# Kernel tuning notes

Measured on AMD Instinct MI355X. Metric: run time of the kernel, lower is better.

The kernel has to match this reference:

```python
import jax, jax.numpy as jnp
import numpy as np

WS = 8      # window size
NH = 8      # num heads
ED = 256    # embed dim
HD = ED // NH  # head dim


def conv2d(x, w, b):
    # x: [B,C,H,W], w: [O,I,3,3] (torch OIHW), SAME padding, stride 1
    y = jax.lax.conv_general_dilated(x, w, (1, 1), 'SAME',
                                     dimension_numbers=('NCHW', 'OIHW', 'NCHW'))
    return y + b[None, :, None, None]


def linear(x, w, b):
    # torch Linear: y = x @ W^T + b, w: [out,in]
    return jnp.einsum('bnc,oc->bno', x, w) + b


def window_partition(x, ws):
    B, C, H, W = x.shape
    x = x.reshape(B, C, H // ws, ws, W // ws, ws)
    x = jnp.transpose(x, (0, 2, 4, 3, 5, 1))  # B, H/ws, W/ws, ws, ws, C
    return x.reshape(-1, ws * ws, C)


def window_reverse(win, H, W, ws, C):
    nW = (H // ws) * (W // ws)
    B = win.shape[0] // nW
    x = win.reshape(B, H // ws, W // ws, ws, ws, C)
    x = jnp.transpose(x, (0, 5, 1, 3, 2, 4))
    return x.reshape(B, C, H, W)


def setup_inputs() -> dict:
    key = jax.random.key(0)
    ks = jax.random.split(key, 24)
    s = 0.02
    inp = {
        'xmap': jax.random.normal(ks[0], (4, ED, 256, 256), jnp.float32),
        'xfeat': jax.random.normal(ks[1], (4, 32, 256, 256), jnp.float32),
        'cmap_w': jax.random.normal(ks[2], (ED, ED, 3, 3), jnp.float32) * s,
        'cmap_b': jnp.zeros((ED,), jnp.float32),
        'cfeat_w': jax.random.normal(ks[3], (ED, 32, 3, 3), jnp.float32) * s,
        'cfeat_b': jnp.zeros((ED,), jnp.float32),
        'qxmap_w': jax.random.normal(ks[4], (ED, ED), jnp.float32) * s,
        'qxmap_b': jnp.zeros((ED,), jnp.float32),
        'kxmap_w': jax.random.normal(ks[5], (ED, ED), jnp.float32) * s,
        'kxmap_b': jnp.zeros((ED,), jnp.float32),
        'vxmap_w': jax.random.normal(ks[6], (ED, ED), jnp.float32) * s,
        'vxmap_b': jnp.zeros((ED,), jnp.float32),
        'qxfeat_w': jax.random.normal(ks[7], (ED, ED), jnp.float32) * s,
        'qxfeat_b': jnp.zeros((ED,), jnp.float32),
        'kxfeat_w': jax.random.normal(ks[8], (ED, ED), jnp.float32) * s,
        'kxfeat_b': jnp.zeros((ED,), jnp.float32),
        'proj_w': jax.random.normal(ks[9], (ED, ED), jnp.float32) * s,
        'proj_b': jnp.zeros((ED,), jnp.float32),
        'cout_w': jax.random.normal(ks[10], (ED, ED, 3, 3), jnp.float32) * s,
        'cout_b': jnp.zeros((ED,), jnp.float32),
    }
    return inp


def reference(xmap, xfeat, cmap_w, cmap_b, cfeat_w, cfeat_b,
              qxmap_w, qxmap_b, kxmap_w, kxmap_b, vxmap_w, vxmap_b,
              qxfeat_w, qxfeat_b, kxfeat_w, kxfeat_b,
              proj_w, proj_b, cout_w, cout_b):
    B, C, H, W = xmap.shape  # xfeat matches spatial size -> no interpolate branch
    xmap = conv2d(xmap, cmap_w, cmap_b)
    identity = xmap
    wm = window_partition(xmap, WS)                        # [Bw, N, C]
    wf = window_partition(conv2d(xfeat, cfeat_w, cfeat_b), WS)
    Bw, N, _ = wm.shape

    def heads(t):
        return jnp.transpose(t.reshape(Bw, N, NH, HD), (0, 2, 1, 3))  # [Bw,H,N,D]

    q_m = heads(linear(wm, qxmap_w, qxmap_b))
    k_m = heads(linear(wm, kxmap_w, kxmap_b))
    v_m = heads(linear(wm, vxmap_w, vxmap_b))
    q_f = heads(linear(wf, qxfeat_w, qxfeat_b))
    k_f = heads(linear(wf, kxfeat_w, kxfeat_b))

    q_g = jax.nn.sigmoid(q_f) * q_m
    k_g = jax.nn.sigmoid(k_f) * k_m

    scale = 1.0 / jnp.sqrt(jnp.asarray(HD, q_g.dtype))
    attn = jax.nn.softmax(jnp.einsum('bhnd,bhmd->bhnm', q_g, k_g) * scale, axis=-1)
    out = jnp.einsum('bhnm,bhmd->bhnd', attn, v_m)         # [Bw,H,N,D]
    out = jnp.transpose(out, (0, 2, 1, 3)).reshape(Bw, N, C)
    out = window_reverse(linear(out, proj_w, proj_b), H, W, WS, C)
    return conv2d(out, cout_w, cout_b) + identity
```

## Files before the change

kernel.cpp:

```cpp
#include <hip/hip_runtime.h>
#include <hip/hip_bf16.h>
#include <cstdint>
#include <math.h>

using bf16 = __hip_bfloat16;
typedef __attribute__((ext_vector_type(4))) float f32x4;
typedef __attribute__((ext_vector_type(8))) short s16x8;
typedef __attribute__((ext_vector_type(4))) short s16x4;

#define AS3(p) ((__attribute__((address_space(3))) void *)(p))
#define AS1(p) ((const __attribute__((address_space(1))) void *)(p))

static constexpr int Himg = 256, Wimg = 256, Bimg = 4;
static constexpr int HWimg = Himg * Wimg;
static constexpr int Ttok = Bimg * HWimg;

__device__ __forceinline__ void gld16(bf16* lds, const bf16* g) {
  __builtin_amdgcn_global_load_lds(AS1(g), AS3(lds), 16, 0, 0);
}

__device__ __forceinline__ unsigned short f2u(float f) {
  bf16 b = __float2bfloat16(f);
  unsigned short u; __builtin_memcpy(&u, &b, 2); return u;
}

__device__ __forceinline__ int remap_lin(int bid, int total) {
  return (bid & 7) * (total >> 3) + (bid >> 3);
}
__device__ __forceinline__ void remap_tile(int bid, int total, int NY, int BMv, int& t0, int& n0) {
  int lin = remap_lin(bid, total);
  t0 = (lin / NY) * BMv;
  n0 = (lin % NY) * 128;
}

__global__ void k_zero4k(float* p) {
  p[blockIdx.x * 256 + threadIdx.x] = 0.f;
}

__global__ void k_castf2b(const float* __restrict__ s, bf16* __restrict__ d, int n) {
  int i = blockIdx.x * 256 + threadIdx.x;
  if (i < n) d[i] = __float2bfloat16(s[i]);
}

__global__ void k_copyf(const float* __restrict__ s, float* __restrict__ d, int n) {
  int i = blockIdx.x * 256 + threadIdx.x;
  if (i < n) d[i] = s[i];
}

__global__ void k_permconv(const float* __restrict__ w, bf16* __restrict__ o, int I) {
  int idx = blockIdx.x * 256 + threadIdx.x;
  int tot = 256 * 9 * I;
  if (idx >= tot) return;
  int i   = idx % I;
  int rem = idx / I;
  int tap = rem % 9;
  int oc  = rem / 9;
  o[idx] = __float2bfloat16(w[(oc * I + i) * 9 + tap]);
}

__global__ void k_tohwc(const float* __restrict__ src, bf16* __restrict__ dst, int C) {
  int bh = blockIdx.x;
  int w0 = blockIdx.y * 32;
  int c0 = blockIdx.z * 32;
  int b = bh / Himg, h = bh % Himg;
  __shared__ float tile[32][33];
  int tid = threadIdx.x;
  int x = tid & 31, y = tid >> 5;
  const float* sp = src + (size_t)b * C * HWimg + (size_t)h * Wimg;
#pragma unroll
  for (int p = 0; p < 4; ++p) {
    int cl = y + p * 8;
    tile[cl][x] = sp[(size_t)(c0 + cl) * HWimg + w0 + x];
  }
  __syncthreads();
#pragma unroll
  for (int p = 0; p < 4; ++p) {
    int wl = y + p * 8;
    dst[((size_t)bh * Wimg + w0 + wl) * C + c0 + x] = __float2bfloat16(tile[x][wl]);
  }
}

template <int TAPS, int EPI>
__global__ void __launch_bounds__(512, 1)
k_gemm8(const bf16* __restrict__ Ain, const bf16* __restrict__ BT,
        const float* __restrict__ bias,
        bf16* __restrict__ outb, int ldo, float* __restrict__ outf,
        const bf16* __restrict__ ident,
        const bf16* __restrict__ zp)
{
  constexpr int KTOT = TAPS * 256;
  const int t0 = remap_lin(blockIdx.x, gridDim.x) * 256;
  const int tid  = threadIdx.x;
  const int wave = tid >> 6, lane = tid & 63;
  const int wr = wave >> 2, wc = wave & 3;
  const int fr = lane & 15, fq = lane >> 4;

  __shared__ __attribute__((aligned(16))) char arena[132608];
  bf16* A0k0 = (bf16*)(arena);
  bf16* A0k1 = (bf16*)(arena + 16384);
  bf16* A1k0 = (bf16*)(arena + 32768);
  bf16* A1k1 = (bf16*)(arena + 49152);
  bf16* B0k0 = (bf16*)(arena + 65536);
  bf16* B0k1 = (bf16*)(arena + 81920);
  bf16* B1k0 = (bf16*)(arena + 98304);
  bf16* B1k1 = (bf16*)(arena + 114688);

  f32x4 acc[8][4] = {};
  s16x8 bfr[4];

  const int slot8 = (fq ^ ((fr >> 1) & 3)) * 8;
  const int aoff  = (wr * 128 + fr) * 32 + slot8;
  const int boff  = (wc * 64 + fr) * 32 + slot8;
  const int ldsl  = (tid & 3) * 8;
  const int scol  = ((tid & 3) ^ ((tid >> 3) & 3)) * 8;
  const int srow  = tid >> 2;

  const bf16* Bb0 = BT + (size_t)srow * KTOT + scol;
  const bf16* Bb1 = BT + (size_t)(128 + srow) * KTOT + scol;
  const bf16* Aa0 = Ain + (size_t)(t0 + srow) * 256 + scol;
  const bf16* Aa1 = Ain + (size_t)(t0 + 128 + srow) * 256 + scol;
  const bf16 *a0c = Aa0, *a1c = Aa1, *a0n = Aa0, *a1n = Aa1;
  const int hU = (t0 >> 8) & 255;

  auto mkbase = [&](int tap, const bf16*& o0, const bf16*& o1) {
    const int dy = tap / 3 - 1, dx = tap % 3 - 1;
    const bool rowok = ((unsigned)(hU + dy)) < 256u;
    const long gb = (long)t0 + dy * Wimg + dx;
    o0 = (rowok && (unsigned)(srow + dx) < 256u)
             ? Ain + (gb + srow) * 256 + scol : zp + scol;
    o1 = (rowok && (unsigned)(128 + srow + dx) < 256u)
             ? Ain + (gb + 128 + srow) * 256 + scol : zp + scol;
  };

#define STA8(DST, P0, P1, CE) do {                                              \
    gld16(DST + srow * 32 + ldsl, (P0) + (CE));                                 \
    gld16(DST + (128 + srow) * 32 + ldsl, (P1) + (CE));                         \
  } while (0)
#define STB8(DST, KE) do {                                                      \
    gld16(DST + srow * 32 + ldsl, Bb0 + (KE));                                  \
    gld16(DST + (128 + srow) * 32 + ldsl, Bb1 + (KE));                          \
  } while (0)

#define NVMs
#define VM4 asm volatile("s_waitcnt vmcnt(4)" ::: "memory")
#define VM0 asm volatile("s_waitcnt vmcnt(0)" ::: "memory")

#define PHO(RA, RB, MH, READB, ...) do {                                         \
    s16x8 af_[4];                                                                \
    _Pragma("unroll") for (int q_ = 0; q_ < 4; ++q_)                             \
      af_[q_] = *(const s16x8*)((RA) + aoff + ((MH) * 4 + q_) * 512);            \
    if (READB) {                                                                 \
      _Pragma("unroll") for (int n_ = 0; n_ < 4; ++n_)                           \
        bfr[n_] = *(const s16x8*)((RB) + boff + n_ * 512);                       \
    }                                                                            \
    __VA_ARGS__;                                                                 \
    asm volatile("s_waitcnt lgkmcnt(0)" ::: "memory");                           \
    __builtin_amdgcn_sched_barrier(0);                                           \
    __builtin_amdgcn_s_setprio(1);                                               \
    _Pragma("unroll") for (int q_ = 0; q_ < 4; ++q_)                             \
      _Pragma("unroll") for (int n_ = 0; n_ < 4; ++n_)                           \
        acc[(MH) * 4 + q_][n_] = __builtin_amdgcn_mfma_f32_16x16x32_bf16(        \
            af_[q_], bfr[n_], acc[(MH) * 4 + q_][n_], 0, 0, 0);                  \
    __builtin_amdgcn_s_setprio(0);                                               \
  } while (0)

#define PHE(RA, RB, MH, READB, VMSTMT, ...) do {                                 \
    s16x8 af_[4];                                                                \
    _Pragma("unroll") for (int q_ = 0; q_ < 4; ++q_)                             \
      af_[q_] = *(const s16x8*)((RA) + aoff + ((MH) * 4 + q_) * 512);            \
    if (READB) {                                                                 \
      _Pragma("unroll") for (int n_ = 0; n_ < 4; ++n_)                           \
        bfr[n_] = *(const s16x8*)((RB) + boff + n_ * 512);                       \
    }                                                                            \
    __VA_ARGS__;                                                                 \
    VMSTMT;                                                                      \
    __builtin_amdgcn_sched_barrier(0);                                           \
    __builtin_amdgcn_s_barrier();                                                \
    asm volatile("s_waitcnt lgkmcnt(0)" ::: "memory");                           \
    __builtin_amdgcn_sched_barrier(0);                                           \
    __builtin_amdgcn_s_setprio(1);                                               \
    _Pragma("unroll") for (int q_ = 0; q_ < 4; ++q_)                             \
      _Pragma("unroll") for (int n_ = 0; n_ < 4; ++n_)                           \
        acc[(MH) * 4 + q_][n_] = __builtin_amdgcn_mfma_f32_16x16x32_bf16(        \
            af_[q_], bfr[n_], acc[(MH) * 4 + q_][n_], 0, 0, 0);                  \
    __builtin_amdgcn_s_setprio(0);                                               \
  } while (0)

  if constexpr (TAPS == 9) {
    mkbase(0, a0c, a1c);
    mkbase(1, a0n, a1n);
    STA8(A0k0, a0c, a1c, 0);  STB8(B0k0, 0);
    STA8(A0k1, a0c, a1c, 32); STB8(B0k1, 32);
    VM4;
    __builtin_amdgcn_s_barrier();
#pragma unroll 1
    for (int tap = 0; tap < 8; ++tap) {
      PHO(A0k0, B0k0, 0, 1, STA8(A1k0, a0c, a1c, 64));
      PHE(A0k0, B0k0, 1, 0, VM4, STB8(B1k0, 64));
      PHO(A0k1, B0k1, 0, 1, STA8(A1k1, a0c, a1c, 96));
      PHE(A0k1, B0k1, 1, 0, VM4, STB8(B1k1, 96));
      PHO(A1k0, B1k0, 0, 1, STA8(A0k0, a0c, a1c, 128));
      PHE(A1k0, B1k0, 1, 0, VM4, STB8(B0k0, 128));
      PHO(A1k1, B1k1, 0, 1, STA8(A0k1, a0c, a1c, 160));
      PHE(A1k1, B1k1, 1, 0, VM4, STB8(B0k1, 160));
      PHO(A0k0, B0k0, 0, 1, STA8(A1k0, a0c, a1c, 192));
      PHE(A0k0, B0k0, 1, 0, VM4, STB8(B1k0, 192));
      PHO(A0k1, B0k1, 0, 1, STA8(A1k1, a0c, a1c, 224));
      PHE(A0k1, B0k1, 1, 0, VM4, STB8(B1k1, 224));
      PHO(A1k0, B1k0, 0, 1, STA8(A0k0, a0n, a1n, 0));
      PHE(A1k0, B1k0, 1, 0, VM4, STB8(B0k0, 256));
      PHO(A1k1, B1k1, 0, 1, STA8(A0k1, a0n, a1n, 32));
      PHE(A1k1, B1k1, 1, 0, VM4, STB8(B0k1, 288));
      a0c = a0n; a1c = a1n;
      if (tap + 2 < 9) mkbase(tap + 2, a0n, a1n);
      Bb0 += 256; Bb1 += 256;
    }
    PHO(A0k0, B0k0, 0, 1, STA8(A1k0, a0c, a1c, 64));
    PHE(A0k0, B0k0, 1, 0, VM4, STB8(B1k0, 64));
    PHO(A0k1, B0k1, 0, 1, STA8(A1k1, a0c, a1c, 96));
    PHE(A0k1, B0k1, 1, 0, VM4, STB8(B1k1, 96));
    PHO(A1k0, B1k0, 0, 1, STA8(A0k0, a0c, a1c, 128));
    PHE(A1k0, B1k0, 1, 0, VM4, STB8(B0k0, 128));
    PHO(A1k1, B1k1, 0, 1, STA8(A0k1, a0c, a1c, 160));
    PHE(A1k1, B1k1, 1, 0, VM4, STB8(B0k1, 160));
    PHO(A0k0, B0k0, 0, 1, STA8(A1k0, a0c, a1c, 192));
    PHE(A0k0, B0k0, 1, 0, VM4, STB8(B1k0, 192));
    PHO(A0k1, B0k1, 0, 1, STA8(A1k1, a0c, a1c, 224));
    PHE(A0k1, B0k1, 1, 0, VM4, STB8(B1k1, 224));
    PHO(A1k0, B1k0, 0, 1, );
    PHE(A1k0, B1k0, 1, 0, VM0, );
    PHO(A1k1, B1k1, 0, 1, );
    PHE(A1k1, B1k1, 1, 0, NVMs, );
  } else {
    STA8(A0k0, Aa0, Aa1, 0);  STB8(B0k0, 0);
    STA8(A0k1, Aa0, Aa1, 32); STB8(B0k1, 32);
    VM4;
    __builtin_amdgcn_s_barrier();
    PHO(A0k0, B0k0, 0, 1, STA8(A1k0, Aa0, Aa1, 64));
    PHE(A0k0, B0k0, 1, 0, VM4, STB8(B1k0, 64));
    PHO(A0k1, B0k1, 0, 1, STA8(A1k1, Aa0, Aa1, 96));
    PHE(A0k1, B0k1, 1, 0, VM4, STB8(B1k1, 96));
    PHO(A1k0, B1k0, 0, 1, STA8(A0k0, Aa0, Aa1, 128));
    PHE(A1k0, B1k0, 1, 0, VM4, STB8(B0k0, 128));
    PHO(A1k1, B1k1, 0, 1, STA8(A0k1, Aa0, Aa1, 160));
    PHE(A1k1, B1k1, 1, 0, VM4, STB8(B0k1, 160));
    PHO(A0k0, B0k0, 0, 1, STA8(A1k0, Aa0, Aa1, 192));
    PHE(A0k0, B0k0, 1, 0, VM4, STB8(B1k0, 192));
    PHO(A0k1, B0k1, 0, 1, STA8(A1k1, Aa0, Aa1, 224));
    PHE(A0k1, B0k1, 1, 0, VM4, STB8(B1k1, 224));
    PHO(A1k0, B1k0, 0, 1, );
    PHE(A1k0, B1k0, 1, 0, VM0, );
    PHO(A1k1, B1k1, 0, 1, );
    PHE(A1k1, B1k1, 1, 0, NVMs, );
  }
#undef PHO
#undef PHE
#undef STA8
#undef STB8
#undef NVMs
#undef VM4
#undef VM0

  if (EPI == 2) {
    float* TR = (float*)arena;
    const int bN = t0 >> 16, hN = (t0 >> 8) & 255;
#pragma unroll 1
    for (int chunk = 0; chunk < 2; ++chunk) {
      __builtin_amdgcn_s_barrier();
      if ((wc >> 1) == chunk) {
#pragma unroll
        for (int m = 0; m < 8; ++m)
#pragma unroll
          for (int n = 0; n < 4; ++n) {
            const int col = wc * 64 + n * 16 + fr;
            const int cl  = (wc & 1) * 64 + n * 16 + fr;
            const float bb = bias[col];
#pragma unroll
            for (int j = 0; j < 4; ++j) {
              const int row = wr * 128 + m * 16 + fq * 4 + j;
              const size_t t = (size_t)t0 + row;
              TR[cl * 259 + row] = acc[m][n][j] + bb +
                                   __bfloat162float(ident[t * 256 + col]);
            }
          }
      }
      __builtin_amdgcn_s_barrier();
      {
        const int cl = tid >> 2, wo = (tid & 3) * 4;
        const int c = chunk * 128 + cl;
        float* dp = outf + (((size_t)bN * 256 + c) * 256 + hN) * 256;
#pragma unroll
        for (int q = 0; q < 16; ++q)
          *(f32x4*)(dp + wo + q * 16) = *(const f32x4*)&TR[cl * 259 + wo + q * 16];
      }
    }
    return;
  }

#pragma unroll
  for (int m = 0; m < 8; ++m) {
#pragma unroll
    for (int n = 0; n < 4; ++n) {
      const int col = wc * 64 + n * 16 + fr;
#pragma unroll
      for (int j = 0; j < 4; ++j) {
        const int row = wr * 128 + m * 16 + fq * 4 + j;
        const size_t t = (size_t)t0 + row;
        outb[t * ldo + col] = __float2bfloat16(acc[m][n][j] + bias[col]);
      }
    }
  }
}

template <int CIN, int TAPS, int EPI>
__global__ void __launch_bounds__(256, 2)
k_gemm(const bf16* __restrict__ Ain, const bf16* __restrict__ BT,
       const float* __restrict__ bias,
       bf16* __restrict__ outb, int ldo,
       const bf16* __restrict__ ident,
       const bf16* __restrict__ zp, int NY)
{
  constexpr int KTOT = TAPS * CIN;
  constexpr int NK = KTOT / 32;
  int t0, n0;
  remap_tile(blockIdx.x, gridDim.x, NY, 256, t0, n0);
  const int tid = threadIdx.x;
  const int wave = tid >> 6, lane = tid & 63;
  const int seg = lane & 3;
  const int rr  = lane >> 2;

  __shared__ bf16 sA0[256 * 32];
  __shared__ bf16 sA1[256 * 32];
  __shared__ bf16 sA2[256 * 32];
  __shared__ bf16 sB0[128 * 32];
  __shared__ bf16 sB1[128 * 32];
  __shared__ bf16 sB2[128 * 32];

  f32x4 acc[8][4] = {};

  const int wr = wave >> 1, wc = wave & 1;
  const int fr = lane & 15, fq = lane >> 4;
  const int sseg = (seg ^ ((rr >> 1) & 3)) * 8;
  const int slot = (fq ^ ((fr >> 1) & 3)) * 8;

#define STAGE(WA, WB, KSV) do {                                                 \
    const int k0_ = (KSV) * 32;                                                 \
    const int tap_ = k0_ / CIN;                                                 \
    const int c0_ = k0_ - tap_ * CIN;                                           \
    const int dy_ = tap_ / 3 - 1, dx_ = tap_ % 3 - 1;                           \
    _Pragma("unroll") for (int i_ = 0; i_ < 4; ++i_) {                          \
      const int g_ = i_ * 4 + wave;                                             \
      const int t_ = t0 + g_ * 16 + rr;                                         \
      const bf16* src_;                                                         \
      if (TAPS == 1) {                                                          \
        src_ = Ain + (size_t)t_ * CIN + k0_ + sseg;                             \
      } else {                                                                  \
        const int hh_ = ((t_ >> 8) & 255) + dy_, ww_ = (t_ & 255) + dx_;        \
        const bool v_ = ((unsigned)hh_ < 256u) && ((unsigned)ww_ < 256u);       \
        const long gi_ = (long)t_ + dy_ * Wimg + dx_;                           \
        src_ = v_ ? (Ain + gi_ * CIN + c0_ + sseg) : (zp + sseg);               \
      }                                                                         \
      gld16(WA + g_ * 16 * 32, src_);                                           \
    }                                                                           \
    _Pragma("unroll") for (int i_ = 0; i_ < 2; ++i_) {                          \
      const int g_ = i_ * 4 + wave;                                             \
      gld16(WB + g_ * 16 * 32,                                                  \
            BT + (size_t)(n0 + g_ * 16 + rr) * KTOT + k0_ + sseg);              \
    }                                                                           \
  } while (0)

#define GSTEP(RA, RB, WA, WB, KSV, LASTF) do {                                  \
    if (LASTF) { asm volatile("s_waitcnt vmcnt(0)" ::: "memory"); }             \
    else       { asm volatile("s_waitcnt vmcnt(6)" ::: "memory"); }             \
    __builtin_amdgcn_s_barrier();                                               \
    s16x8 af_[8], bf_[4];                                                       \
    _Pragma("unroll") for (int m_ = 0; m_ < 8; ++m_)                            \
      af_[m_] = *(const s16x8*)(RA + (wr * 128 + m_ * 16 + fr) * 32 + slot);    \
    _Pragma("unroll") for (int n_ = 0; n_ < 4; ++n_)                            \
      bf_[n_] = *(const s16x8*)(RB + (wc * 64 + n_ * 16 + fr) * 32 + slot);     \
    if ((KSV) + 2 < NK) STAGE(WA, WB, (KSV) + 2);                               \
    __builtin_amdgcn_s_setprio(1);                                              \
    _Pragma("unroll") for (int m_ = 0; m_ < 8; ++m_)                            \
      _Pragma("unroll") for (int n_ = 0; n_ < 4; ++n_)                          \
        acc[m_][n_] = __builtin_amdgcn_mfma_f32_16x16x32_bf16(af_[m_], bf_[n_], acc[m_][n_], 0, 0, 0); \
    __builtin_amdgcn_s_setprio(0);                                              \
  } while (0)

  STAGE(sA0, sB0, 0);
  STAGE(sA1, sB1, 1);

  constexpr int NMAIN = ((NK - 1) / 3) * 3;
  int ks = 0;
#pragma unroll 1
  for (; ks < NMAIN; ks += 3) {
    GSTEP(sA0, sB0, sA2, sB2, ks,     false);
    GSTEP(sA1, sB1, sA0, sB0, ks + 1, false);
    GSTEP(sA2, sB2, sA1, sB1, ks + 2, false);
  }
  constexpr int TREM = NK - NMAIN;
  if constexpr (TREM == 3) {
    GSTEP(sA0, sB0, sA2, sB2, NMAIN,     false);
    GSTEP(sA1, sB1, sA0, sB0, NMAIN + 1, false);
    GSTEP(sA2, sB2, sA1, sB1, NMAIN + 2, true);
  } else if constexpr (TREM == 2) {
    GSTEP(sA0, sB0, sA2, sB2, NMAIN,     false);
    GSTEP(sA1, sB1, sA0, sB0, NMAIN + 1, true);
  } else {
    GSTEP(sA0, sB0, sA2, sB2, NMAIN,     true);
  }
#undef GSTEP
#undef STAGE

#pragma unroll
  for (int m = 0; m < 8; ++m) {
#pragma unroll
    for (int n = 0; n < 4; ++n) {
      const int col = n0 + wc * 64 + n * 16 + fr;
#pragma unroll
      for (int j = 0; j < 4; ++j) {
        const int row = wr * 128 + m * 16 + fq * 4 + j;
        const size_t t = (size_t)t0 + row;
        float v = acc[m][n][j] + bias[col];
        if (EPI == 0) {
          outb[t * ldo + col] = __float2bfloat16(v);
        } else {
          v += __bfloat162float(ident[t * 256 + col]);
          outb[t * 256 + col] = __float2bfloat16(v);
        }
      }
    }
  }
}

__global__ void __launch_bounds__(256, 2)
k_gemm_qkv(const bf16* __restrict__ Am, const bf16* __restrict__ Af,
           const bf16* __restrict__ Bm, const bf16* __restrict__ Bf,
           const float* __restrict__ bm, const float* __restrict__ bfi,
           bf16* __restrict__ out)
{
  int t0, n0;
  remap_tile(blockIdx.x, gridDim.x, 4, 128, t0, n0);
  const int tid = threadIdx.x;
  const int wave = tid >> 6, lane = tid & 63;
  const int seg = lane & 3;
  const int rr  = lane >> 2;

  __shared__ bf16 sA0[128 * 32];
  __shared__ bf16 sA1[128 * 32];
  __shared__ bf16 sA2[128 * 32];
  __shared__ bf16 sB0[128 * 32];
  __shared__ bf16 sB1[128 * 32];
  __shared__ bf16 sB2[128 * 32];

  f32x4 accm[4][4] = {};
  f32x4 accf[4][4] = {};

  const int wr = wave >> 1, wc = wave & 1;
  const int fr = lane & 15, fq = lane >> 4;
  const int sseg = (seg ^ ((rr >> 1) & 3)) * 8;
  const int slot = (fq ^ ((fr >> 1) & 3)) * 8;

#define STAGEQ(WA, WB, SV) do {                                                 \
    const int k0_ = ((SV) >> 1) * 32;                                           \
    const bf16* A_ = ((SV) & 1) ? Af : Am;                                      \
    const bf16* B_ = ((SV) & 1) ? Bf : Bm;                                      \
    _Pragma("unroll") for (int i_ = 0; i_ < 2; ++i_) {                          \
      const int r_ = wave * 32 + i_ * 16 + rr;                                  \
      gld16(WA + (wave * 32 + i_ * 16) * 32, A_ + (size_t)(t0 + r_) * 256 + k0_ + sseg); \
      gld16(WB + (wave * 32 + i_ * 16) * 32, B_ + (size_t)(n0 + r_) * 256 + k0_ + sseg); \
    }                                                                           \
  } while (0)

#define QSTEP(RA, RB, WA, WB, SV, LASTF) do {                                   \
    if (LASTF) { asm volatile("s_waitcnt vmcnt(0)" ::: "memory"); }             \
    else       { asm volatile("s_waitcnt vmcnt(4)" ::: "memory"); }             \
    __builtin_amdgcn_s_barrier();                                               \
    s16x8 af_[4], bf_[4];                                                       \
    _Pragma("unroll") for (int m_ = 0; m_ < 4; ++m_)                            \
      af_[m_] = *(const s16x8*)(RA + (wr * 64 + m_ * 16 + fr) * 32 + slot);     \
    _Pragma("unroll") for (int n_ = 0; n_ < 4; ++n_)                            \
      bf_[n_] = *(const s16x8*)(RB + (wc * 64 + n_ * 16 + fr) * 32 + slot);     \
    if ((SV) + 2 < 16) STAGEQ(WA, WB, (SV) + 2);                                \
    __builtin_amdgcn_s_setprio(1);                                              \
    if ((SV) & 1) {                                                             \
      _Pragma("unroll") for (int m_ = 0; m_ < 4; ++m_)                          \
        _Pragma("unroll") for (int n_ = 0; n_ < 4; ++n_)                        \
          accf[m_][n_] = __builtin_amdgcn_mfma_f32_16x16x32_bf16(af_[m_], bf_[n_], accf[m_][n_], 0, 0, 0); \
    } else {                                                                    \
      _Pragma("unroll") for (int m_ = 0; m_ < 4; ++m_)                          \
        _Pragma("unroll") for (int n_ = 0; n_ < 4; ++n_)                        \
          accm[m_][n_] = __builtin_amdgcn_mfma_f32_16x16x32_bf16(af_[m_], bf_[n_], accm[m_][n_], 0, 0, 0); \
    }                                                                           \
    __builtin_amdgcn_s_setprio(0);                                              \
  } while (0)

  STAGEQ(sA0, sB0, 0);
  STAGEQ(sA1, sB1, 1);

  int s = 0;
#pragma unroll 1
  for (; s < 15; s += 3) {
    QSTEP(sA0, sB0, sA2, sB2, s,     false);
    QSTEP(sA1, sB1, sA0, sB0, s + 1, false);
    QSTEP(sA2, sB2, sA1, sB1, s + 2, false);
  }
  QSTEP(sA0, sB0, sA2, sB2, 15, true);
#undef QSTEP
#undef STAGEQ

#pragma unroll
  for (int m = 0; m < 4; ++m) {
#pragma unroll
    for (int n = 0; n < 4; ++n) {
      const int col = n0 + wc * 64 + n * 16 + fr;
#pragma unroll
      for (int j = 0; j < 4; ++j) {
        const int row = wr * 64 + m * 16 + fq * 4 + j;
        const size_t t = (size_t)t0 + row;
        float v = accm[m][n][j] + bm[col];
        const float g = accf[m][n][j] + bfi[col];
        v *= 1.f / (1.f + __expf(-g));
        out[t * 768 + col] = __float2bfloat16(v);
      }
    }
  }
}

__global__ void __launch_bounds__(256, 2)
k_attn_mfma(const bf16* __restrict__ qkv, bf16* __restrict__ out) {
  __shared__ short smem[4 * 7424];
  const int tid = threadIdx.x;
  const int wave = tid >> 6, lane = tid & 63;
  const int fr = lane & 15, fq = lane >> 4;
  const int wi = blockIdx.x >> 1;
  const int head = (blockIdx.x & 1) * 4 + wave;
  const int b = wi >> 10, rem = wi & 1023, wh = rem >> 5, ww = rem & 31;
  const size_t tbase = (size_t)b * HWimg + (size_t)(wh * 8) * Wimg + ww * 8;

  short* Qs = smem + wave * 7424;
  short* Ks = Qs + 2560;
  short* VT = Qs + 5120;
  short* P  = Qs;
  short* Ol = Qs;

  auto tok = [&](int i) -> size_t {
    return tbase + (size_t)(i >> 3) * Wimg + (i & 7);
  };

  {
    const bf16* tb = qkv + tok(lane) * 768 + head * 32;
#pragma unroll
    for (int c = 0; c < 4; ++c) {
      s16x8 qv = *(const s16x8*)(tb + c * 8);
      s16x8 kv = *(const s16x8*)(tb + 256 + c * 8);
      s16x8 vv = *(const s16x8*)(tb + 512 + c * 8);
      *(s16x8*)(Qs + lane * 40 + c * 8) = qv;
      *(s16x8*)(Ks + lane * 40 + c * 8) = kv;
#pragma unroll
      for (int e = 0; e < 8; ++e) VT[(c * 8 + e) * 72 + lane] = vv[e];
    }
  }

  s16x8 kf[4], qf[4];
#pragma unroll
  for (int m = 0; m < 4; ++m)
    kf[m] = *(const s16x8*)(Ks + (fr + 16 * m) * 40 + fq * 8);
#pragma unroll
  for (int n = 0; n < 4; ++n)
    qf[n] = *(const s16x8*)(Qs + (fr + 16 * n) * 40 + fq * 8);

  f32x4 st[4][4] = {};
#pragma unroll
  for (int m = 0; m < 4; ++m)
#pragma unroll
    for (int n = 0; n < 4; ++n)
      st[m][n] = __builtin_amdgcn_mfma_f32_16x16x32_bf16(kf[m], qf[n], st[m][n], 0, 0, 0);

  const float scale = 0.17677669529663688f;
  float invs[4];
#pragma unroll
  for (int n = 0; n < 4; ++n) {
    float mx = -1e30f;
#pragma unroll
    for (int m = 0; m < 4; ++m)
#pragma unroll
      for (int j = 0; j < 4; ++j) mx = fmaxf(mx, st[m][n][j]);
    mx = fmaxf(mx, __shfl_xor(mx, 16));
    mx = fmaxf(mx, __shfl_xor(mx, 32));
    float sum = 0.f;
#pragma unroll
    for (int m = 0; m < 4; ++m) {
      s16x4 pk;
#pragma unroll
      for (int j = 0; j < 4; ++j) {
        float e = __expf((st[m][n][j] - mx) * scale);
        sum += e;
        pk[j] = (short)f2u(e);
      }
      *(s16x4*)(P + (fr + 16 * n) * 72 + 16 * m + 4 * fq) = pk;
    }
    sum += __shfl_xor(sum, 16);
    sum += __shfl_xor(sum, 32);
    invs[n] = 1.f / sum;
  }

  f32x4 oc[4][2] = {};
#pragma unroll
  for (int ks = 0; ks < 2; ++ks) {
    s16x8 pf[4], vf[2];
#pragma unroll
    for (int m = 0; m < 4; ++m)
      pf[m] = *(const s16x8*)(P + (fr + 16 * m) * 72 + ks * 32 + fq * 8);
#pragma unroll
    for (int n = 0; n < 2; ++n)
      vf[n] = *(const s16x8*)(VT + (fr + 16 * n) * 72 + ks * 32 + fq * 8);
#pragma unroll
    for (int m = 0; m < 4; ++m)
#pragma unroll
      for (int n = 0; n < 2; ++n)
        oc[m][n] = __builtin_amdgcn_mfma_f32_16x16x32_bf16(pf[m], vf[n], oc[m][n], 0, 0, 0);
  }

#pragma unroll
  for (int m = 0; m < 4; ++m)
#pragma unroll
    for (int j = 0; j < 4; ++j) {
      const float inv = __shfl(invs[m], 4 * fq + j);
      const int q = 16 * m + 4 * fq + j;
#pragma unroll
      for (int n = 0; n < 2; ++n)
        Ol[q * 40 + fr + 16 * n] = (short)f2u(oc[m][n][j] * inv);
    }
  {
    bf16* op = out + tok(lane) * 256 + head * 32;
#pragma unroll
    for (int c = 0; c < 4; ++c)
      *(s16x8*)(op + c * 8) = *(const s16x8*)(Ol + lane * 40 + c * 8);
  }
}

extern "C" void kernel_launch(void* const* d_in, const int* in_sizes, int n_in,
                              void* d_out, int out_size, void* d_ws, size_t ws_size,
                              hipStream_t stream) {
  const float* xmap    = (const float*)d_in[0];
  const float* xfeat   = (const float*)d_in[1];
  const float* cmap_w  = (const float*)d_in[2];
  const float* cmap_b  = (const float*)d_in[3];
  const float* cfeat_w = (const float*)d_in[4];
  const float* cfeat_b = (const float*)d_in[5];
  const float* qxmap_w = (const float*)d_in[6];
  const float* qxmap_b = (const float*)d_in[7];
  const float* kxmap_w = (const float*)d_in[8];
  const float* kxmap_b = (const float*)d_in[9];
  const float* vxmap_w = (const float*)d_in[10];
  const float* vxmap_b = (const float*)d_in[11];
  const float* qxfeat_w = (const float*)d_in[12];
  const float* qxfeat_b = (const float*)d_in[13];
  const float* kxfeat_w = (const float*)d_in[14];
  const float* kxfeat_b = (const float*)d_in[15];
  const float* proj_w  = (const float*)d_in[16];
  const float* proj_b  = (const float*)d_in[17];
  const float* cout_w  = (const float*)d_in[18];
  const float* cout_b  = (const float*)d_in[19];

  uint8_t* ws = (uint8_t*)d_ws;
  size_t off = 0;
  auto alloc = [&](size_t bytes) -> void* {
    void* p = ws + off;
    off += (bytes + 255) & ~(size_t)255;
    return p;
  };
  float* zp       = (float*)alloc(4096);
  bf16* cmap_wT   = (bf16*)alloc((size_t)2304 * 256 * 2);
  bf16* cout_wT   = (bf16*)alloc((size_t)2304 * 256 * 2);
  bf16* cfeat_wT  = (bf16*)alloc((size_t)288 * 256 * 2);
  bf16* lin_qkv_wT= (bf16*)alloc((size_t)768 * 256 * 2);
  bf16* lin_f_wT  = (bf16*)alloc((size_t)512 * 256 * 2);
  bf16* proj_wT   = (bf16*)alloc((size_t)256 * 256 * 2);
  float* bias_qkv = (float*)alloc(768 * 4);
  float* bias_f   = (float*)alloc(512 * 4);
  bf16* xm_nhwc   = (bf16*)alloc((size_t)Ttok * 256 * 2);
  bf16* xf_nhwc   = (bf16*)alloc((size_t)Ttok * 32 * 2);
  bf16* xc        = (bf16*)alloc((size_t)Ttok * 256 * 2);
  bf16* fc        = (bf16*)alloc((size_t)Ttok * 256 * 2);
  bf16* qkv       = (bf16*)alloc((size_t)Ttok * 768 * 2);
  bf16* attn_out  = xm_nhwc;
  bf16* proj_out  = fc;
  bf16* zpb = (bf16*)zp;

  k_zero4k<<<4, 256, 0, stream>>>(zp);
  k_permconv<<<(256 * 9 * 256 + 255) / 256, 256, 0, stream>>>(cmap_w, cmap_wT, 256);
  k_permconv<<<(256 * 9 * 256 + 255) / 256, 256, 0, stream>>>(cout_w, cout_wT, 256);
  k_permconv<<<(256 * 9 * 32 + 255) / 256, 256, 0, stream>>>(cfeat_w, cfeat_wT, 32);
  k_castf2b<<<256, 256, 0, stream>>>(qxmap_w, lin_qkv_wT, 65536);
  k_castf2b<<<256, 256, 0, stream>>>(kxmap_w, lin_qkv_wT + 65536, 65536);
  k_castf2b<<<256, 256, 0, stream>>>(vxmap_w, lin_qkv_wT + 131072, 65536);
  k_castf2b<<<256, 256, 0, stream>>>(qxfeat_w, lin_f_wT, 65536);
  k_castf2b<<<256, 256, 0, stream>>>(kxfeat_w, lin_f_wT + 65536, 65536);
  k_castf2b<<<256, 256, 0, stream>>>(proj_w, proj_wT, 65536);
  k_copyf<<<1, 256, 0, stream>>>(qxmap_b, bias_qkv, 256);
  k_copyf<<<1, 256, 0, stream>>>(kxmap_b, bias_qkv + 256, 256);
  k_copyf<<<1, 256, 0, stream>>>(vxmap_b, bias_qkv + 512, 256);
  k_copyf<<<1, 256, 0, stream>>>(qxfeat_b, bias_f, 256);
  k_copyf<<<1, 256, 0, stream>>>(kxfeat_b, bias_f + 256, 256);

  k_tohwc<<<dim3(Bimg * Himg, Wimg / 32, 256 / 32), 256, 0, stream>>>(xmap, xm_nhwc, 256);
  k_tohwc<<<dim3(Bimg * Himg, Wimg / 32, 1), 256, 0, stream>>>(xfeat, xf_nhwc, 32);

  const int NB = Ttok / 256;
  k_gemm8<9, 0><<<dim3(NB), dim3(512), 0, stream>>>(
      xm_nhwc, cmap_wT, cmap_b, xc, 256, nullptr, nullptr, zpb);
  k_gemm<32, 9, 0><<<dim3(NB * 2), dim3(256), 0, stream>>>(
      xf_nhwc, cfeat_wT, cfeat_b, fc, 256, nullptr, zpb, 2);
  k_gemm8<1, 0><<<dim3(NB), dim3(512), 0, stream>>>(
      xc, lin_qkv_wT + 131072, bias_qkv + 512, qkv + 512, 768, nullptr, nullptr, zpb);
  k_gemm_qkv<<<dim3((Ttok / 128) * 4), dim3(256), 0, stream>>>(
      xc, fc, lin_qkv_wT, lin_f_wT, bias_qkv, bias_f, qkv);
  k_attn_mfma<<<dim3(4096 * 2), dim3(256), 0, stream>>>(qkv, attn_out);
  k_gemm8<1, 0><<<dim3(NB), dim3(512), 0, stream>>>(
      attn_out, proj_wT, proj_b, proj_out, 256, nullptr, nullptr, zpb);
  k_gemm8<9, 2><<<dim3(NB), dim3(512), 0, stream>>>(
      proj_out, cout_wT, cout_b, nullptr, 0, (float*)d_out, xc, zpb);
}
```

Measured before the change: 1.396 ms.

## Rewrite gated QK GEMM as 512-thread 256x128 tile with quad-buffered phased pipeline

Replaces the 256-thread 128x128-tile gated Q/K projection kernel with a 512-thread kernel that computes a 256x128 output tile per block. It uses four LDS buffers and a fully unrolled two-phase schedule per stage, with explicit waitcnt and sched barriers so global-to-LDS loads overlap MFMA work. The goal is more reuse of each loaded weight tile and fewer barriers per step. The cost is more LDS, larger per-wave accumulators and one block per CU, which may limit latency hiding.

```diff
diff --git a/kernel.cpp b/kernel.cpp
--- a/kernel.cpp
+++ b/kernel.cpp
@@ -432,90 +432,146 @@
   }
 }
 
-__global__ void __launch_bounds__(256, 2)
-k_gemm_qkv(const bf16* __restrict__ Am, const bf16* __restrict__ Af,
-           const bf16* __restrict__ Bm, const bf16* __restrict__ Bf,
-           const float* __restrict__ bm, const float* __restrict__ bfi,
-           bf16* __restrict__ out)
+__global__ void __launch_bounds__(512, 1)
+k_gemm_qkv8(const bf16* __restrict__ Am, const bf16* __restrict__ Af,
+            const bf16* __restrict__ Bm, const bf16* __restrict__ Bf,
+            const float* __restrict__ bm, const float* __restrict__ bfi,
+            bf16* __restrict__ out)
 {
-  int t0, n0;
-  remap_tile(blockIdx.x, gridDim.x, 4, 128, t0, n0);
-  const int tid = threadIdx.x;
+  const int lin = remap_lin(blockIdx.x, gridDim.x);
+  const int t0 = (lin >> 2) * 256;
+  const int n0 = (lin & 3) * 128;
+  const int tid  = threadIdx.x;
   const int wave = tid >> 6, lane = tid & 63;
-  const int seg = lane & 3;
-  const int rr  = lane >> 2;
-
-  __shared__ bf16 sA0[128 * 32];
-  __shared__ bf16 sA1[128 * 32];
-  __shared__ bf16 sA2[128 * 32];
-  __shared__ bf16 sB0[128 * 32];
-  __shared__ bf16 sB1[128 * 32];
-  __shared__ bf16 sB2[128 * 32];
-
-  f32x4 accm[4][4] = {};
-  f32x4 accf[4][4] = {};
-
-  const int wr = wave >> 1, wc = wave & 1;
+  const int wr = wave >> 2, wc = wave & 3;
   const int fr = lane & 15, fq = lane >> 4;
-  const int sseg = (seg ^ ((rr >> 1) & 3)) * 8;
-  const int slot = (fq ^ ((fr >> 1) & 3)) * 8;
-
-#define STAGEQ(WA, WB, SV) do {                                                 \
-    const int k0_ = ((SV) >> 1) * 32;                                           \
-    const bf16* A_ = ((SV) & 1) ? Af : Am;                                      \
-    const bf16* B_ = ((SV) & 1) ? Bf : Bm;                                      \
-    _Pragma("unroll") for (int i_ = 0; i_ < 2; ++i_) {                          \
-      const int r_ = wave * 32 + i_ * 16 + rr;                                  \
-      gld16(WA + (wave * 32 + i_ * 16) * 32, A_ + (size_t)(t0 + r_) * 256 + k0_ + sseg); \
-      gld16(WB + (wave * 32 + i_ * 16) * 32, B_ + (size_t)(n0 + r_) * 256 + k0_ + sseg); \
-    }                                                                           \
-  } while (0)
-
-#define QSTEP(RA, RB, WA, WB, SV, LASTF) do {                                   \
-    if (LASTF) { asm volatile("s_waitcnt vmcnt(0)" ::: "memory"); }             \
-    else       { asm volatile("s_waitcnt vmcnt(4)" ::: "memory"); }             \
+
+  __shared__ bf16 AS0[256 * 32];
+  __shared__ bf16 AS1[256 * 32];
+  __shared__ bf16 AS2[256 * 32];
+  __shared__ bf16 AS3[256 * 32];
+  __shared__ bf16 BS0[128 * 32];
+  __shared__ bf16 BS1[128 * 32];
+  __shared__ bf16 BS2[128 * 32];
+  __shared__ bf16 BS3[128 * 32];
+
+  f32x4 accm[8][2] = {};
+  f32x4 accf[8][2] = {};
+  s16x8 bfr[2];
+
+  const int slot8 = (fq ^ ((fr >> 1) & 3)) * 8;
+  const int aoff  = (wr * 128 + fr) * 32 + slot8;
+  const int boffq = (wc * 32 + fr) * 32 + slot8;
+  const int ldsl  = (tid & 3) * 8;
+  const int scol  = ((tid & 3) ^ ((tid >> 3) & 3)) * 8;
+  const int srow  = tid >> 2;
+
+  const bf16* am0 = Am + (size_t)(t0 + srow) * 256 + scol;
+  const bf16* am1 = Am + (size_t)(t0 + 128 + srow) * 256 + scol;
+  const bf16* af0 = Af + (size_t)(t0 + srow) * 256 + scol;
+  const bf16* af1 = Af + (size_t)(t0 + 128 + srow) * 256 + scol;
+  const bf16* bmB = Bm + (size_t)(n0 + srow) * 256 + scol;
+  const bf16* bfB = Bf + (size_t)(n0 + srow) * 256 + scol;
+
+#define STAQ(DST, P0, P1, KE) do {                                              \
+    gld16(DST + srow * 32 + ldsl, (P0) + (KE));                                 \
+    gld16(DST + (128 + srow) * 32 + ldsl, (P1) + (KE));                         \
+  } while (0)
+#define STBQ(DST, PB, KE) gld16(DST + srow * 32 + ldsl, (PB) + (KE))
+
+#define NVMs
+#define VM3 asm volatile("s_waitcnt vmcnt(3)" ::: "memory")
+#define VM0 asm volatile("s_waitcnt vmcnt(0)" ::: "memory")
+
+#define PHOQ(RA, RB, ACC, ...) do {                                             \
+    s16x8 af_[4];                                                               \
+    _Pragma("unroll") for (int q_ = 0; q_ < 4; ++q_)                            \
+      af_[q_] = *(const s16x8*)((RA) + aoff + q_ * 512);                        \
+    _Pragma("unroll") for (int n_ = 0; n_ < 2; ++n_)                            \
+      bfr[n_] = *(const s16x8*)((RB) + boffq + n_ * 512);                       \
+    __VA_ARGS__;                                                                \
+    asm volatile("s_waitcnt lgkmcnt(0)" ::: "memory");                          \
+    __builtin_amdgcn_sched_barrier(0);                                          \
+    __builtin_amdgcn_s_setprio(1);                                              \
+    _Pragma("unroll") for (int q_ = 0; q_ < 4; ++q_)                            \
+      _Pragma("unroll") for (int n_ = 0; n_ < 2; ++n_)                          \
+        ACC[q_][n_] = __builtin_amdgcn_mfma_f32_16x16x32_bf16(                  \
+            af_[q_], bfr[n_], ACC[q_][n_], 0, 0, 0);                            \
+    __builtin_amdgcn_s_setprio(0);                                              \
+  } while (0)
+
+#define PHEQ(RA, ACC, VMSTMT, ...) do {                                         \
+    s16x8 af_[4];                                                               \
+    _Pragma("unroll") for (int q_ = 0; q_ < 4; ++q_)                            \
+      af_[q_] = *(const s16x8*)((RA) + aoff + (4 + q_) * 512);                  \
+    __VA_ARGS__;                                                                \
+    VMSTMT;                                                                     \
+    __builtin_amdgcn_sched_barrier(0);                                          \
     __builtin_amdgcn_s_barrier();                                               \
-    s16x8 af_[4], bf_[4];                                                       \
-    _Pragma("unroll") for (int m_ = 0; m_ < 4; ++m_)                            \
-      af_[m_] = *(const s16x8*)(RA + (wr * 64 + m_ * 16 + fr) * 32 + slot);     \
-    _Pragma("unroll") for (int n_ = 0; n_ < 4; ++n_)                            \
-      bf_[n_] = *(const s16x8*)(RB + (wc * 64 + n_ * 16 + fr) * 32 + slot);     \
-    if ((SV) + 2 < 16) STAGEQ(WA, WB, (SV) + 2);                                \
+    asm volatile("s_waitcnt lgkmcnt(0)" ::: "memory");                          \
+    __builtin_amdgcn_sched_barrier(0);                                          \
     __builtin_amdgcn_s_setprio(1);                                              \
-    if ((SV) & 1) {                                                             \
-      _Pragma("unroll") for (int m_ = 0; m_ < 4; ++m_)                          \
-        _Pragma("unroll") for (int n_ = 0; n_ < 4; ++n_)                        \
-          accf[m_][n_] = __builtin_amdgcn_mfma_f32_16x16x32_bf16(af_[m_], bf_[n_], accf[m_][n_], 0, 0, 0); \
-    } else {                                                                    \
-      _Pragma("unroll") for (int m_ = 0; m_ < 4; ++m_)                          \
-        _Pragma("unroll") for (int n_ = 0; n_ < 4; ++n_)                        \
-          accm[m_][n_] = __builtin_amdgcn_mfma_f32_16x16x32_bf16(af_[m_], bf_[n_], accm[m_][n_], 0, 0, 0); \
-    }                                                                           \
+    _Pragma("unroll") for (int q_ = 0; q_ < 4; ++q_)                            \
+      _Pragma("unroll") for (int n_ = 0; n_ < 2; ++n_)                          \
+        ACC[4 + q_][n_] = __builtin_amdgcn_mfma_f32_16x16x32_bf16(              \
+            af_[q_], bfr[n_], ACC[4 + q_][n_], 0, 0, 0);                        \
     __builtin_amdgcn_s_setprio(0);                                              \
   } while (0)
 
-  STAGEQ(sA0, sB0, 0);
-  STAGEQ(sA1, sB1, 1);
-
-  int s = 0;
-#pragma unroll 1
-  for (; s < 15; s += 3) {
-    QSTEP(sA0, sB0, sA2, sB2, s,     false);
-    QSTEP(sA1, sB1, sA0, sB0, s + 1, false);
-    QSTEP(sA2, sB2, sA1, sB1, s + 2, false);
-  }
-  QSTEP(sA0, sB0, sA2, sB2, 15, true);
-#undef QSTEP
-#undef STAGEQ
-
-#pragma unroll
-  for (int m = 0; m < 4; ++m) {
-#pragma unroll
-    for (int n = 0; n < 4; ++n) {
-      const int col = n0 + wc * 64 + n * 16 + fr;
+  STAQ(AS0, am0, am1, 0);  STBQ(BS0, bmB, 0);
+  STAQ(AS1, am0, am1, 32); STBQ(BS1, bmB, 32);
+  VM3;
+  __builtin_amdgcn_s_barrier();
+
+  PHOQ(AS0, BS0, accm, STAQ(AS2, af0, af1, 0));
+  PHEQ(AS0, accm, VM3, STBQ(BS2, bfB, 0));
+  PHOQ(AS1, BS1, accm, STAQ(AS3, af0, af1, 32));
+  PHEQ(AS1, accm, VM3, STBQ(BS3, bfB, 32));
+  PHOQ(AS2, BS2, accf, STAQ(AS0, am0, am1, 64));
+  PHEQ(AS2, accf, VM3, STBQ(BS0, bmB, 64));
+  PHOQ(AS3, BS3, accf, STAQ(AS1, am0, am1, 96));
+  PHEQ(AS3, accf, VM3, STBQ(BS1, bmB, 96));
+  PHOQ(AS0, BS0, accm, STAQ(AS2, af0, af1, 64));
+  PHEQ(AS0, accm, VM3, STBQ(BS2, bfB, 64));
+  PHOQ(AS1, BS1, accm, STAQ(AS3, af0, af1, 96));
+  PHEQ(AS1, accm, VM3, STBQ(BS3, bfB, 96));
+  PHOQ(AS2, BS2, accf, STAQ(AS0, am0, am1, 128));
+  PHEQ(AS2, accf, VM3, STBQ(BS0, bmB, 128));
+  PHOQ(AS3, BS3, accf, STAQ(AS1, am0, am1, 160));
+  PHEQ(AS3, accf, VM3, STBQ(BS1, bmB, 160));
+  PHOQ(AS0, BS0, accm, STAQ(AS2, af0, af1, 128));
+  PHEQ(AS0, accm, VM3, STBQ(BS2, bfB, 128));
+  PHOQ(AS1, BS1, accm, STAQ(AS3, af0, af1, 160));
+  PHEQ(AS1, accm, VM3, STBQ(BS3, bfB, 160));
+  PHOQ(AS2, BS2, accf, STAQ(AS0, am0, am1, 192));
+  PHEQ(AS2, accf, VM3, STBQ(BS0, bmB, 192));
+  PHOQ(AS3, BS3, accf, STAQ(AS1, am0, am1, 224));
+  PHEQ(AS3, accf, VM3, STBQ(BS1, bmB, 224));
+  PHOQ(AS0, BS0, accm, STAQ(AS2, af0, af1, 192));
+  PHEQ(AS0, accm, VM3, STBQ(BS2, bfB, 192));
+  PHOQ(AS1, BS1, accm, STAQ(AS3, af0, af1, 224));
+  PHEQ(AS1, accm, VM3, STBQ(BS3, bfB, 224));
+  PHOQ(AS2, BS2, accf, );
+  PHEQ(AS2, accf, VM0, );
+  PHOQ(AS3, BS3, accf, );
+  PHEQ(AS3, accf, NVMs, );
+
+#undef PHOQ
+#undef PHEQ
+#undef STAQ
+#undef STBQ
+#undef NVMs
+#undef VM3
+#undef VM0
+
+#pragma unroll
+  for (int m = 0; m < 8; ++m) {
+#pragma unroll
+    for (int n = 0; n < 2; ++n) {
+      const int col = n0 + wc * 32 + n * 16 + fr;
 #pragma unroll
       for (int j = 0; j < 4; ++j) {
-        const int row = wr * 64 + m * 16 + fq * 4 + j;
+        const int row = wr * 128 + m * 16 + fq * 4 + j;
         const size_t t = (size_t)t0 + row;
         float v = accm[m][n][j] + bm[col];
         const float g = accf[m][n][j] + bfi[col];
@@ -714,7 +770,7 @@
       xf_nhwc, cfeat_wT, cfeat_b, fc, 256, nullptr, zpb, 2);
   k_gemm8<1, 0><<<dim3(NB), dim3(512), 0, stream>>>(
       xc, lin_qkv_wT + 131072, bias_qkv + 512, qkv + 512, 768, nullptr, nullptr, zpb);
-  k_gemm_qkv<<<dim3((Ttok / 128) * 4), dim3(256), 0, stream>>>(
+  k_gemm_qkv8<<<dim3(NB * 4), dim3(512), 0, stream>>>(
       xc, fc, lin_qkv_wT, lin_f_wT, bias_qkv, bias_f, qkv);
   k_attn_mfma<<<dim3(4096 * 2), dim3(256), 0, stream>>>(qkv, attn_out);
   k_gemm8<1, 0><<<dim3(NB), dim3(512), 0, stream>>>(
```

Result: no change. 1.409 ms (+1.0%).
